# Kernel tuning notes

Hardware: AMD Instinct MI355X
Metric: run time of the kernel (lower is better)

The kernel has to match this reference:

```python
import jax, jax.numpy as jnp
import numpy as np

BETA = 0.9
ADAPT_RATE = 0.1


def _surrogate_spike(x):
    gate = jax.nn.sigmoid(5.0 * x)
    hard = (x > 0).astype(x.dtype)
    return jax.lax.stop_gradient(hard - gate) + gate


def setup_inputs() -> dict:
    key = jax.random.key(0)
    k1, k2, k3, k4, k5 = jax.random.split(key, 5)
    B, T, D, H = 64, 256, 512, 1024
    x = jax.random.normal(k1, (B, T, D), dtype=jnp.float32)
    # fc_in: Linear(D, H); fc_out: Linear(H, 1)
    W_in = jax.random.normal(k2, (H, D), dtype=jnp.float32) * (1.0 / np.sqrt(D))
    b_in = jax.random.normal(k3, (H,), dtype=jnp.float32) * 0.01
    W_out = jax.random.normal(k4, (1, H), dtype=jnp.float32) * (1.0 / np.sqrt(H))
    b_out = jax.random.normal(k5, (1,), dtype=jnp.float32) * 0.01
    return {"x": x, "W_in": W_in, "b_in": b_in, "W_out": W_out, "b_out": b_out}


def reference(x, W_in, b_in, W_out, b_out):
    B, T, D = x.shape
    H = W_in.shape[0]
    # batch fc_in over all timesteps outside the recurrence
    pre = jnp.einsum('btd,hd->bth', x, W_in) + b_in  # [B,T,H]

    def step(carry, p_t):
        mem, adapt = carry
        mem = BETA * mem + p_t - adapt
        spk = _surrogate_spike(mem)
        adapt = adapt + ADAPT_RATE * spk
        mem = mem - spk  # reset_mode == 'subtract'
        return (mem, adapt), spk

    init = (jnp.zeros((B, H), x.dtype), jnp.zeros((B, H), x.dtype))
    _, spks = jax.lax.scan(step, init, jnp.swapaxes(pre, 0, 1))  # spks: [T,B,H]

    # mean_t fc_out(spk_t) == fc_out(mean_t spk_t) since fc_out is affine
    spk_mean = spks.mean(axis=0)  # [B,H]
    return spk_mean @ W_out.T + b_out  # [B,1]
```

## Files before the change

kernel.cpp:

```cpp
#include <hip/hip_runtime.h>

constexpr int Bb = 64;
constexpr int Tt = 256;
constexpr int Dd = 512;
constexpr int Hh = 1024;
constexpr int Mm = Bb * Tt;

typedef _Float16 half8 __attribute__((ext_vector_type(8)));
typedef _Float16 half4v __attribute__((ext_vector_type(4)));
typedef float floatx16 __attribute__((ext_vector_type(16)));

#define GPTR(x) ((const __attribute__((address_space(1))) void*)(x))
#define LPTR(x) ((__attribute__((address_space(3))) void*)(x))

__global__ __launch_bounds__(256) void convert_t(const float* __restrict__ x,
                                                 const float* __restrict__ Win,
                                                 _Float16* __restrict__ xh,
                                                 _Float16* __restrict__ xl,
                                                 _Float16* __restrict__ wh,
                                                 _Float16* __restrict__ wl,
                                                 const float* __restrict__ bout,
                                                 float* __restrict__ out) {
    __shared__ _Float16 lh[64 * 72];
    __shared__ _Float16 ll[64 * 72];
    const int tid = threadIdx.x;
    const int k0 = blockIdx.x * 64;

    if (blockIdx.x == 0 && blockIdx.y == 0 && tid < Bb) out[tid] = bout[0];

    const float* src;
    _Float16 *dh, *dl;
    int nrows, m0;
    if (blockIdx.y < 256) {
        src = x; dh = xh; dl = xl; nrows = Mm; m0 = blockIdx.y * 64;
    } else {
        src = Win; dh = wh; dl = wl; nrows = Hh; m0 = (blockIdx.y - 256) * 64;
    }

#pragma unroll
    for (int i = 0; i < 4; ++i) {
        const int lin = tid + i * 256;
        const int row = lin >> 4;
        const int c4 = (lin & 15) * 4;
        const float4 v = *(const float4*)(src + (size_t)(m0 + row) * Dd + k0 + c4);
        const float va[4] = {v.x, v.y, v.z, v.w};
        half4v h, l;
#pragma unroll
        for (int q = 0; q < 4; ++q) {
            const _Float16 hi = (_Float16)va[q];
            h[q] = hi;
            l[q] = (_Float16)((va[q] - (float)hi) * 4096.0f);
        }
        *(half4v*)&lh[row * 72 + c4] = h;
        *(half4v*)&ll[row * 72 + c4] = l;
    }
    __syncthreads();
#pragma unroll
    for (int i = 0; i < 2; ++i) {
        const int lin = tid + i * 256;
        const int kc = lin >> 6;
        const int mm = lin & 63;
        const half8 h = *(const half8*)&lh[mm * 72 + kc * 8];
        const half8 l = *(const half8*)&ll[mm * 72 + kc * 8];
        const size_t g = (size_t)(k0 / 8 + kc) * nrows + m0 + mm;
        *(half8*)(dh + g * 8) = h;
        *(half8*)(dl + g * 8) = l;
    }
}

__global__ __launch_bounds__(256, 2) void gemm_fused(const _Float16* __restrict__ xh,
                                                     const _Float16* __restrict__ xl,
                                                     const _Float16* __restrict__ wh,
                                                     const _Float16* __restrict__ wl,
                                                     const float* __restrict__ bin,
                                                     const float* __restrict__ Wout,
                                                     float* __restrict__ out) {
    __shared__ float ldsS[16384];
    _Float16* ldsB = (_Float16*)ldsS;

    const int tid = threadIdx.x;
    const int id = blockIdx.x;
    const int j  = id & 7;
    const int q  = id >> 3;
    const int nt = q & 15;
    const int b  = (q >> 4) * 8 + j;
    const int m0 = b * Tt;
    const int n0 = nt * 64;

    const int lane = tid & 63;
    const int wave = tid >> 6;
    const int lr = lane & 31;
    const int lk = lane >> 5;

    floatx16 acc[2][2], accx[2][2];
#pragma unroll
    for (int mi = 0; mi < 2; ++mi)
#pragma unroll
        for (int ni = 0; ni < 2; ++ni)
#pragma unroll
            for (int r = 0; r < 16; ++r) { acc[mi][ni][r] = 0.0f; accx[mi][ni][r] = 0.0f; }

#define STAGE_B(buf, SS)                                                             \
    do {                                                                             \
        _Pragma("unroll")                                                            \
        for (int i_ = 0; i_ < 2; ++i_) {                                             \
            const int c_ = tid + i_ * 256;                                           \
            const int kc_ = c_ >> 6;                                                 \
            const int col_ = c_ & 63;                                                \
            const size_t g_ = ((size_t)((SS) * 8 + kc_) * Hh + n0 + col_) * 8;       \
            __builtin_amdgcn_global_load_lds(GPTR(wh + g_), LPTR(&ldsB[((buf) * 2 + 0) * 4096 + c_ * 8]), 16, 0, 0); \
            __builtin_amdgcn_global_load_lds(GPTR(wl + g_), LPTR(&ldsB[((buf) * 2 + 1) * 4096 + c_ * 8]), 16, 0, 0); \
        }                                                                            \
    } while (0)

    const size_t arow0 = (size_t)(m0 + wave * 64 + lr);
    half8 aset[2][4];
#define LOAD_A(rot, hs)                                                              \
    do {                                                                             \
        const size_t kA = (size_t)((hs) * 2 + lk) * Mm;                              \
        aset[rot][0] = *(const half8*)(xh + (kA + arow0) * 8);                       \
        aset[rot][1] = *(const half8*)(xh + (kA + arow0 + 32) * 8);                  \
        aset[rot][2] = *(const half8*)(xl + (kA + arow0) * 8);                       \
        aset[rot][3] = *(const half8*)(xl + (kA + arow0 + 32) * 8);                  \
    } while (0)

    STAGE_B(0, 0);
    LOAD_A(0, 0);

    for (int SS = 0; SS < 8; ++SS) {
        __syncthreads();
        if (SS < 7) STAGE_B((SS + 1) & 1, SS + 1);
        const int cur = SS & 1;
#pragma unroll
        for (int qq = 0; qq < 4; ++qq) {
            const int hs = SS * 4 + qq;
            const int rot = hs & 1;
            if (hs < 31) LOAD_A(rot ^ 1, hs + 1);

            half8 bh[2], bl[2];
#pragma unroll
            for (int ni = 0; ni < 2; ++ni) {
                const int ci = (qq * 2 + lk) * 64 + ni * 32 + lr;
                bh[ni] = *(const half8*)&ldsB[(cur * 2 + 0) * 4096 + ci * 8];
                bl[ni] = *(const half8*)&ldsB[(cur * 2 + 1) * 4096 + ci * 8];
            }
#pragma unroll
            for (int mi = 0; mi < 2; ++mi)
#pragma unroll
                for (int ni = 0; ni < 2; ++ni) {
                    acc[mi][ni]  = __builtin_amdgcn_mfma_f32_32x32x16_f16(aset[rot][mi],     bh[ni], acc[mi][ni], 0, 0, 0);
                    accx[mi][ni] = __builtin_amdgcn_mfma_f32_32x32x16_f16(aset[rot][mi],     bl[ni], accx[mi][ni], 0, 0, 0);
                    accx[mi][ni] = __builtin_amdgcn_mfma_f32_32x32x16_f16(aset[rot][2 + mi], bh[ni], accx[mi][ni], 0, 0, 0);
                }
        }
    }
#undef STAGE_B
#undef LOAD_A

    __syncthreads();
    float* scanbuf = ldsS;

#pragma unroll
    for (int p = 0; p < 2; ++p) {
        const float bv = bin[n0 + p * 32 + lr];
#pragma unroll
        for (int mi = 0; mi < 2; ++mi)
#pragma unroll
            for (int r = 0; r < 16; ++r) {
                const int row = (r & 3) + 8 * (r >> 2) + 4 * lk;
                const int t = wave * 64 + mi * 32 + row;
                scanbuf[p * 8192 + t * 32 + lr] =
                    acc[mi][p][r] + accx[mi][p][r] * (1.0f / 4096.0f) + bv;
            }
    }
    __syncthreads();

    if (wave == 0) {
        const float* sb = scanbuf + (lane >> 5) * 8192 + (lane & 31);
        float mem = 0.0f, adapt = 0.0f, cnt = 0.0f;
#pragma unroll 8
        for (int t = 0; t < Tt; ++t) {
            const float v = sb[t * 32];
            mem = 0.9f * mem + v - adapt;
            const float spk = (mem > 0.0f) ? 1.0f : 0.0f;
            adapt += 0.1f * spk;
            mem -= spk;
            cnt += spk;
        }
        float val = cnt * Wout[n0 + lane] * (1.0f / (float)Tt);
#pragma unroll
        for (int off = 32; off > 0; off >>= 1) val += __shfl_down(val, off, 64);
        if (lane == 0) atomicAdd(&out[b], val);
    }
}

#define BK 16
#define BMP 132
__global__ __launch_bounds__(256) void gemm_pre(const float* __restrict__ x,
                                                const float* __restrict__ Win,
                                                const float* __restrict__ bin,
                                                float* __restrict__ pre) {
    __shared__ float As[BK][BMP];
    __shared__ float Bs[BK][BMP];
    const int tid = threadIdx.x;
    const int m0 = blockIdx.y * 128;
    const int n0 = blockIdx.x * 128;
    const int tx = tid & 15;
    const int ty = tid >> 4;
    float acc[8][8];
#pragma unroll
    for (int i = 0; i < 8; ++i)
#pragma unroll
        for (int jj = 0; jj < 8; ++jj) acc[i][jj] = 0.0f;
    const float* Aptr = x + (size_t)m0 * Dd;
    const float* Bptr = Win + (size_t)n0 * Dd;
    for (int k0 = 0; k0 < Dd; k0 += BK) {
#pragma unroll
        for (int i = 0; i < 2; ++i) {
            const int lin = tid + i * 256;
            const int row = lin >> 2;
            const int kq = (lin & 3) << 2;
            const float4 av = *(const float4*)(Aptr + (size_t)row * Dd + k0 + kq);
            const float4 bv = *(const float4*)(Bptr + (size_t)row * Dd + k0 + kq);
            As[kq + 0][row] = av.x; As[kq + 1][row] = av.y;
            As[kq + 2][row] = av.z; As[kq + 3][row] = av.w;
            Bs[kq + 0][row] = bv.x; Bs[kq + 1][row] = bv.y;
            Bs[kq + 2][row] = bv.z; Bs[kq + 3][row] = bv.w;
        }
        __syncthreads();
#pragma unroll
        for (int kk = 0; kk < BK; ++kk) {
            const float4 a0 = *(const float4*)&As[kk][ty * 4];
            const float4 a1 = *(const float4*)&As[kk][ty * 4 + 64];
            const float4 b0 = *(const float4*)&Bs[kk][tx * 4];
            const float4 b1 = *(const float4*)&Bs[kk][tx * 4 + 64];
            const float a[8] = {a0.x, a0.y, a0.z, a0.w, a1.x, a1.y, a1.z, a1.w};
            const float b[8] = {b0.x, b0.y, b0.z, b0.w, b1.x, b1.y, b1.z, b1.w};
#pragma unroll
            for (int i = 0; i < 8; ++i)
#pragma unroll
                for (int jj = 0; jj < 8; ++jj) acc[i][jj] += a[i] * b[jj];
        }
        __syncthreads();
    }
#pragma unroll
    for (int i = 0; i < 8; ++i) {
        const int m = m0 + ((i < 4) ? (ty * 4 + i) : (64 + ty * 4 + i - 4));
#pragma unroll
        for (int half = 0; half < 2; ++half) {
            const int n = n0 + tx * 4 + half * 64;
            float4 v;
            v.x = acc[i][half * 4 + 0] + bin[n + 0];
            v.y = acc[i][half * 4 + 1] + bin[n + 1];
            v.z = acc[i][half * 4 + 2] + bin[n + 2];
            v.w = acc[i][half * 4 + 3] + bin[n + 3];
            *(float4*)(pre + (size_t)m * Hh + n) = v;
        }
    }
}

__global__ __launch_bounds__(64) void init_out(const float* __restrict__ bout,
                                               float* __restrict__ out) {
    out[threadIdx.x] = bout[0];
}

__global__ __launch_bounds__(64) void alif_scan(const float* __restrict__ pre,
                                                const float* __restrict__ Wout,
                                                float* __restrict__ out) {
    const int h = blockIdx.x * 64 + threadIdx.x;
    const int b = blockIdx.y;
    const float* p = pre + (size_t)b * Tt * Hh + h;

    float buf[32];
#pragma unroll
    for (int jj = 0; jj < 32; ++jj) buf[jj] = p[(size_t)jj * Hh];

    float mem = 0.0f, adapt = 0.0f, cnt = 0.0f;
    for (int t0 = 0; t0 < Tt; t0 += 32) {
        float cur[32];
#pragma unroll
        for (int jj = 0; jj < 32; ++jj) cur[jj] = buf[jj];
        if (t0 + 32 < Tt) {
#pragma unroll
            for (int jj = 0; jj < 32; ++jj) buf[jj] = p[(size_t)(t0 + 32 + jj) * Hh];
        }
#pragma unroll
        for (int jj = 0; jj < 32; ++jj) {
            mem = 0.9f * mem + cur[jj] - adapt;
            const float spk = (mem > 0.0f) ? 1.0f : 0.0f;
            adapt += 0.1f * spk;
            mem -= spk;
            cnt += spk;
        }
    }

    float val = cnt * Wout[h] * (1.0f / (float)Tt);
#pragma unroll
    for (int off = 32; off > 0; off >>= 1) val += __shfl_down(val, off, 64);
    if (threadIdx.x == 0) atomicAdd(&out[b], val);
}

extern "C" void kernel_launch(void* const* d_in, const int* in_sizes, int n_in,
                              void* d_out, int out_size, void* d_ws, size_t ws_size,
                              hipStream_t stream) {
    const float* x    = (const float*)d_in[0];
    const float* Win  = (const float*)d_in[1];
    const float* bin  = (const float*)d_in[2];
    const float* Wout = (const float*)d_in[3];
    const float* bout = (const float*)d_in[4];
    float* out = (float*)d_out;

    const size_t xh_bytes = (size_t)Mm * Dd * 2;
    const size_t wh_bytes = (size_t)Hh * Dd * 2;
    const size_t need = 2 * xh_bytes + 2 * wh_bytes + 4096;

    if (ws_size >= need) {
        char* base = (char*)d_ws;
        _Float16* xh = (_Float16*)base;
        _Float16* xl = (_Float16*)(base + xh_bytes);
        _Float16* wh = (_Float16*)(base + 2 * xh_bytes);
        _Float16* wl = (_Float16*)(base + 2 * xh_bytes + wh_bytes);

        convert_t<<<dim3(8, 272), 256, 0, stream>>>(x, Win, xh, xl, wh, wl, bout, out);

        gemm_fused<<<1024, 256, 0, stream>>>(xh, xl, wh, wl, bin, Wout, out);
    } else {
        float* pre = (float*)d_ws;
        init_out<<<1, 64, 0, stream>>>(bout, out);
        dim3 g1(Hh / 128, Mm / 128);
        gemm_pre<<<g1, 256, 0, stream>>>(x, Win, bin, pre);
        alif_scan<<<dim3(Hh / 64, Bb), 64, 0, stream>>>(pre, Wout, out);
    }
}
```

Before: 144.7 us.

## Shrink fused GEMM tile to 32 columns with 8 waves of 32 rows

Each fused GEMM+scan block now covers one batch's 256 timesteps by 32 hidden units instead of 64, using 8 waves that each own a 32x32 MFMA tile rather than 4 waves with 2x2 tiles. The grid doubles to 2048 blocks, LDS use halves and launch bounds rise to 512 threads, aiming for more parallelism, occupancy and fewer registers per thread. In exchange every A fragment of x is loaded twice as often across blocks (less register-level reuse), and the serial scan uses only 32 lanes per block.

```diff
diff --git a/kernel.cpp b/kernel.cpp
--- a/kernel.cpp
+++ b/kernel.cpp
@@ -68,60 +68,53 @@
     }
 }
 
-__global__ __launch_bounds__(256, 2) void gemm_fused(const _Float16* __restrict__ xh,
+__global__ __launch_bounds__(512, 4) void gemm_fused(const _Float16* __restrict__ xh,
                                                      const _Float16* __restrict__ xl,
                                                      const _Float16* __restrict__ wh,
                                                      const _Float16* __restrict__ wl,
                                                      const float* __restrict__ bin,
                                                      const float* __restrict__ Wout,
                                                      float* __restrict__ out) {
-    __shared__ float ldsS[16384];
+    __shared__ float ldsS[8192];
     _Float16* ldsB = (_Float16*)ldsS;
 
     const int tid = threadIdx.x;
     const int id = blockIdx.x;
     const int j  = id & 7;
-    const int q  = id >> 3;
-    const int nt = q & 15;
-    const int b  = (q >> 4) * 8 + j;
+    const int s  = id >> 3;
+    const int nt = s & 31;
+    const int b  = (s >> 5) * 8 + j;
     const int m0 = b * Tt;
-    const int n0 = nt * 64;
+    const int n0 = nt * 32;
 
     const int lane = tid & 63;
     const int wave = tid >> 6;
     const int lr = lane & 31;
     const int lk = lane >> 5;
 
-    floatx16 acc[2][2], accx[2][2];
-#pragma unroll
-    for (int mi = 0; mi < 2; ++mi)
-#pragma unroll
-        for (int ni = 0; ni < 2; ++ni)
-#pragma unroll
-            for (int r = 0; r < 16; ++r) { acc[mi][ni][r] = 0.0f; accx[mi][ni][r] = 0.0f; }
-
+    floatx16 acc, accx;
+#pragma unroll
+    for (int r = 0; r < 16; ++r) { acc[r] = 0.0f; accx[r] = 0.0f; }
+
+    const int sb_arr = tid >> 8;
+    const int sb_c8  = tid & 255;
+    const int sb_kc  = sb_c8 >> 5;
+    const int sb_col = sb_c8 & 31;
+    const _Float16* sb_src = sb_arr ? wl : wh;
 #define STAGE_B(buf, SS)                                                             \
     do {                                                                             \
-        _Pragma("unroll")                                                            \
-        for (int i_ = 0; i_ < 2; ++i_) {                                             \
-            const int c_ = tid + i_ * 256;                                           \
-            const int kc_ = c_ >> 6;                                                 \
-            const int col_ = c_ & 63;                                                \
-            const size_t g_ = ((size_t)((SS) * 8 + kc_) * Hh + n0 + col_) * 8;       \
-            __builtin_amdgcn_global_load_lds(GPTR(wh + g_), LPTR(&ldsB[((buf) * 2 + 0) * 4096 + c_ * 8]), 16, 0, 0); \
-            __builtin_amdgcn_global_load_lds(GPTR(wl + g_), LPTR(&ldsB[((buf) * 2 + 1) * 4096 + c_ * 8]), 16, 0, 0); \
-        }                                                                            \
+        const size_t g_ = ((size_t)((SS) * 8 + sb_kc) * Hh + n0 + sb_col) * 8;       \
+        __builtin_amdgcn_global_load_lds(GPTR(sb_src + g_),                          \
+            LPTR(&ldsB[(((buf) * 2 + sb_arr) * 256 + sb_c8) * 8]), 16, 0, 0);        \
     } while (0)
 
-    const size_t arow0 = (size_t)(m0 + wave * 64 + lr);
-    half8 aset[2][4];
+    const size_t arow = (size_t)(m0 + wave * 32 + lr);
+    half8 aset[2][2];
 #define LOAD_A(rot, hs)                                                              \
     do {                                                                             \
-        const size_t kA = (size_t)((hs) * 2 + lk) * Mm;                              \
-        aset[rot][0] = *(const half8*)(xh + (kA + arow0) * 8);                       \
-        aset[rot][1] = *(const half8*)(xh + (kA + arow0 + 32) * 8);                  \
-        aset[rot][2] = *(const half8*)(xl + (kA + arow0) * 8);                       \
-        aset[rot][3] = *(const half8*)(xl + (kA + arow0 + 32) * 8);                  \
+        const size_t kA = ((size_t)((hs) * 2 + lk) * Mm + arow) * 8;                 \
+        aset[rot][0] = *(const half8*)(xh + kA);                                     \
+        aset[rot][1] = *(const half8*)(xl + kA);                                     \
     } while (0)
 
     STAGE_B(0, 0);
@@ -137,21 +130,13 @@
             const int rot = hs & 1;
             if (hs < 31) LOAD_A(rot ^ 1, hs + 1);
 
-            half8 bh[2], bl[2];
-#pragma unroll
-            for (int ni = 0; ni < 2; ++ni) {
-                const int ci = (qq * 2 + lk) * 64 + ni * 32 + lr;
-                bh[ni] = *(const half8*)&ldsB[(cur * 2 + 0) * 4096 + ci * 8];
-                bl[ni] = *(const half8*)&ldsB[(cur * 2 + 1) * 4096 + ci * 8];
-            }
-#pragma unroll
-            for (int mi = 0; mi < 2; ++mi)
-#pragma unroll
-                for (int ni = 0; ni < 2; ++ni) {
-                    acc[mi][ni]  = __builtin_amdgcn_mfma_f32_32x32x16_f16(aset[rot][mi],     bh[ni], acc[mi][ni], 0, 0, 0);
-                    accx[mi][ni] = __builtin_amdgcn_mfma_f32_32x32x16_f16(aset[rot][mi],     bl[ni], accx[mi][ni], 0, 0, 0);
-                    accx[mi][ni] = __builtin_amdgcn_mfma_f32_32x32x16_f16(aset[rot][2 + mi], bh[ni], accx[mi][ni], 0, 0, 0);
-                }
+            const int ci = (qq * 2 + lk) * 32 + lr;
+            const half8 bh = *(const half8*)&ldsB[((cur * 2 + 0) * 256 + ci) * 8];
+            const half8 bl = *(const half8*)&ldsB[((cur * 2 + 1) * 256 + ci) * 8];
+
+            acc  = __builtin_amdgcn_mfma_f32_32x32x16_f16(aset[rot][0], bh, acc,  0, 0, 0);
+            accx = __builtin_amdgcn_mfma_f32_32x32x16_f16(aset[rot][0], bl, accx, 0, 0, 0);
+            accx = __builtin_amdgcn_mfma_f32_32x32x16_f16(aset[rot][1], bh, accx, 0, 0, 0);
         }
     }
 #undef STAGE_B
@@ -160,23 +145,17 @@
     __syncthreads();
     float* scanbuf = ldsS;
 
-#pragma unroll
-    for (int p = 0; p < 2; ++p) {
-        const float bv = bin[n0 + p * 32 + lr];
-#pragma unroll
-        for (int mi = 0; mi < 2; ++mi)
-#pragma unroll
-            for (int r = 0; r < 16; ++r) {
-                const int row = (r & 3) + 8 * (r >> 2) + 4 * lk;
-                const int t = wave * 64 + mi * 32 + row;
-                scanbuf[p * 8192 + t * 32 + lr] =
-                    acc[mi][p][r] + accx[mi][p][r] * (1.0f / 4096.0f) + bv;
-            }
+    const float bv = bin[n0 + lr];
+#pragma unroll
+    for (int r = 0; r < 16; ++r) {
+        const int row = (r & 3) + 8 * (r >> 2) + 4 * lk;
+        const int t = wave * 32 + row;
+        scanbuf[t * 32 + lr] = acc[r] + accx[r] * (1.0f / 4096.0f) + bv;
     }
     __syncthreads();
 
-    if (wave == 0) {
-        const float* sb = scanbuf + (lane >> 5) * 8192 + (lane & 31);
+    if (wave == 0 && lane < 32) {
+        const float* sb = scanbuf + lane;
         float mem = 0.0f, adapt = 0.0f, cnt = 0.0f;
 #pragma unroll 8
         for (int t = 0; t < Tt; ++t) {
@@ -189,7 +168,7 @@
         }
         float val = cnt * Wout[n0 + lane] * (1.0f / (float)Tt);
 #pragma unroll
-        for (int off = 32; off > 0; off >>= 1) val += __shfl_down(val, off, 64);
+        for (int off = 16; off > 0; off >>= 1) val += __shfl_down(val, off, 32);
         if (lane == 0) atomicAdd(&out[b], val);
     }
 }
@@ -323,7 +302,7 @@
 
         convert_t<<<dim3(8, 272), 256, 0, stream>>>(x, Win, xh, xl, wh, wl, bout, out);
 
-        gemm_fused<<<1024, 256, 0, stream>>>(xh, xl, wh, wl, bin, Wout, out);
+        gemm_fused<<<2048, 512, 0, stream>>>(xh, xl, wh, wl, bin, Wout, out);
     } else {
         float* pre = (float*)d_ws;
         init_out<<<1, 64, 0, stream>>>(bout, out);
```

Result: slower. 169.1 us (+16.9%).
